# Kernel tuning notes

Hardware: AMD Instinct MI355X
Metric: run time of the kernel (lower is better)

## Reference

```python
import jax, jax.numpy as jnp
import numpy as np
import math

D_DIM = 512
N_HEAD = 8
HIDDEN = 2048
N_LAYERS = 4
CONTEXT = 64
MAX_LEN = 5000


def make_pe(d_model, max_len=MAX_LEN):
    position = np.arange(max_len)[:, None].astype(np.float32)
    div_term = np.exp(np.arange(0, d_model, 2).astype(np.float32) * (-math.log(10000.0) / d_model))
    pe = np.zeros((max_len, d_model), dtype=np.float32)
    pe[:, 0::2] = np.sin(position * div_term)
    pe[:, 1::2] = np.cos(position * div_term)
    return jnp.asarray(pe)


def setup_inputs() -> dict:
    key = jax.random.key(0)
    ks = jax.random.split(key, 64)
    B, T, IN = 16, 2048, 512
    inp = {}
    inp["trajectory"] = jax.random.normal(ks[0], (B, T, IN), dtype=jnp.float32)
    inp["obs_length"] = jax.random.randint(ks[1], (B,), 0, T)
    s = 0.02
    inp["w_in"] = jax.random.normal(ks[2], (IN, D_DIM), dtype=jnp.float32) * s
    inp["b_in"] = jnp.zeros((D_DIM,), dtype=jnp.float32)
    # per-layer params
    params = []
    ki = 3
    for l in range(N_LAYERS):
        p = {}
        p["w_qkv"] = jax.random.normal(ks[ki], (D_DIM, 3 * D_DIM), dtype=jnp.float32) * s; ki += 1
        p["b_qkv"] = jnp.zeros((3 * D_DIM,), dtype=jnp.float32)
        p["w_o"] = jax.random.normal(ks[ki], (D_DIM, D_DIM), dtype=jnp.float32) * s; ki += 1
        p["b_o"] = jnp.zeros((D_DIM,), dtype=jnp.float32)
        p["w_ff1"] = jax.random.normal(ks[ki], (D_DIM, HIDDEN), dtype=jnp.float32) * s; ki += 1
        p["b_ff1"] = jnp.zeros((HIDDEN,), dtype=jnp.float32)
        p["w_ff2"] = jax.random.normal(ks[ki], (HIDDEN, D_DIM), dtype=jnp.float32) * s; ki += 1
        p["b_ff2"] = jnp.zeros((D_DIM,), dtype=jnp.float32)
        p["ln1_g"] = jnp.ones((D_DIM,), dtype=jnp.float32)
        p["ln1_b"] = jnp.zeros((D_DIM,), dtype=jnp.float32)
        p["ln2_g"] = jnp.ones((D_DIM,), dtype=jnp.float32)
        p["ln2_b"] = jnp.zeros((D_DIM,), dtype=jnp.float32)
        for name, v in p.items():
            inp[f"L{l}_{name}"] = v
    return inp


def layer_norm(x, g, b, eps=1e-5):
    mu = jnp.mean(x, axis=-1, keepdims=True)
    var = jnp.mean((x - mu) ** 2, axis=-1, keepdims=True)
    return (x - mu) * jax.lax.rsqrt(var + eps) * g + b


def build_attn_mask(T, obs_length, context_length):
    # boolean mask, True = masked out. Causal + per-sample context window.
    i = jnp.arange(T)[:, None]
    j = jnp.arange(T)[None, :]
    causal = j > i  # (T, T)
    # window restriction applies for rows i with context_length < i < obs_length:
    # mask positions j <= i - context_length - 1, i.e. j < i - context_length
    window = j < (i - context_length)  # (T,T)
    row_active = (i[None, :, :] > context_length) & (i[None, :, :] < obs_length[:, None, None])  # (B,T,1)
    mask = causal[None] | (window[None] & row_active)  # (B,T,T)
    return mask


def encoder_layer(x, mask_add, pad_bool, p):
    B, T, D = x.shape
    H = N_HEAD
    Dh = D // H
    qkv = x @ p["w_qkv"] + p["b_qkv"]  # (B,T,3D)
    q, k, v = jnp.split(qkv, 3, axis=-1)
    q = q.reshape(B, T, H, Dh).transpose(0, 2, 1, 3)
    k = k.reshape(B, T, H, Dh).transpose(0, 2, 1, 3)
    v = v.reshape(B, T, H, Dh).transpose(0, 2, 1, 3)
    scores = jnp.einsum("bhqd,bhkd->bhqk", q, k) / jnp.sqrt(jnp.float32(Dh))
    scores = scores + mask_add[:, None] + pad_bool[:, None, None, :] * jnp.float32(-1e9)
    attn = jax.nn.softmax(scores, axis=-1)
    ctx = jnp.einsum("bhqk,bhkd->bhqd", attn, v)
    ctx = ctx.transpose(0, 2, 1, 3).reshape(B, T, D)
    attn_out = ctx @ p["w_o"] + p["b_o"]
    x = layer_norm(x + attn_out, p["ln1_g"], p["ln1_b"])
    ff = jax.nn.relu(x @ p["w_ff1"] + p["b_ff1"]) @ p["w_ff2"] + p["b_ff2"]
    x = layer_norm(x + ff, p["ln2_g"], p["ln2_b"])
    return x


def reference(trajectory, obs_length, w_in, b_in,
              L0_w_qkv, L0_b_qkv, L0_w_o, L0_b_o, L0_w_ff1, L0_b_ff1, L0_w_ff2, L0_b_ff2, L0_ln1_g, L0_ln1_b, L0_ln2_g, L0_ln2_b,
              L1_w_qkv, L1_b_qkv, L1_w_o, L1_b_o, L1_w_ff1, L1_b_ff1, L1_w_ff2, L1_b_ff2, L1_ln1_g, L1_ln1_b, L1_ln2_g, L1_ln2_b,
              L2_w_qkv, L2_b_qkv, L2_w_o, L2_b_o, L2_w_ff1, L2_b_ff1, L2_w_ff2, L2_b_ff2, L2_ln1_g, L2_ln1_b, L2_ln2_g, L2_ln2_b,
              L3_w_qkv, L3_b_qkv, L3_w_o, L3_b_o, L3_w_ff1, L3_b_ff1, L3_w_ff2, L3_b_ff2, L3_ln1_g, L3_ln1_b, L3_ln2_g, L3_ln2_b):
    B, T, _ = trajectory.shape
    pad = jnp.arange(T)[None, :] > obs_length[:, None]  # (B,T) True = pad
    x = trajectory @ w_in + b_in
    x = x + make_pe(D_DIM)[None, :T]
    mask_bool = build_attn_mask(T, obs_length, CONTEXT)  # (B,T,T)
    mask_add = jnp.where(mask_bool, jnp.float32(-1e9), jnp.float32(0.0))
    layers = [
        dict(w_qkv=L0_w_qkv, b_qkv=L0_b_qkv, w_o=L0_w_o, b_o=L0_b_o, w_ff1=L0_w_ff1, b_ff1=L0_b_ff1, w_ff2=L0_w_ff2, b_ff2=L0_b_ff2, ln1_g=L0_ln1_g, ln1_b=L0_ln1_b, ln2_g=L0_ln2_g, ln2_b=L0_ln2_b),
        dict(w_qkv=L1_w_qkv, b_qkv=L1_b_qkv, w_o=L1_w_o, b_o=L1_b_o, w_ff1=L1_w_ff1, b_ff1=L1_b_ff1, w_ff2=L1_w_ff2, b_ff2=L1_b_ff2, ln1_g=L1_ln1_g, ln1_b=L1_ln1_b, ln2_g=L1_ln2_g, ln2_b=L1_ln2_b),
        dict(w_qkv=L2_w_qkv, b_qkv=L2_b_qkv, w_o=L2_w_o, b_o=L2_b_o, w_ff1=L2_w_ff1, b_ff1=L2_b_ff1, w_ff2=L2_w_ff2, b_ff2=L2_b_ff2, ln1_g=L2_ln1_g, ln1_b=L2_ln1_b, ln2_g=L2_ln2_g, ln2_b=L2_ln2_b),
        dict(w_qkv=L3_w_qkv, b_qkv=L3_b_qkv, w_o=L3_w_o, b_o=L3_b_o, w_ff1=L3_w_ff1, b_ff1=L3_b_ff1, w_ff2=L3_w_ff2, b_ff2=L3_b_ff2, ln1_g=L3_ln1_g, ln1_b=L3_ln1_b, ln2_g=L3_ln2_g, ln2_b=L3_ln2_b),
    ]
    for p in layers:
        x = encoder_layer(x, mask_add, pad, p)
    # aggregate
    keep = ~pad
    x = x * keep[:, :, None]
    denom = jnp.sum(keep, axis=1).astype(x.dtype)[:, None]
    return jnp.sum(x, axis=1) / denom
```

## Files before the change

kernel.cpp:

```cpp
#include <hip/hip_runtime.h>

typedef unsigned short u16;
typedef unsigned int u32;
typedef __bf16 bf16x8 __attribute__((ext_vector_type(8)));
typedef float f32x4 __attribute__((ext_vector_type(4)));

#define MFMA16(a, b, c) __builtin_amdgcn_mfma_f32_16x16x32_bf16((a), (b), (c), 0, 0, 0)

__device__ __forceinline__ u16 f2bf(float x) {
    union { float f; u32 u; } v; v.f = x;
    u32 r = v.u + 0x7fffu + ((v.u >> 16) & 1u);
    return (u16)(r >> 16);
}
__device__ __forceinline__ float bf2f(u16 x) {
    union { u32 u; float f; } v; v.u = ((u32)x) << 16; return v.f;
}

typedef const __attribute__((address_space(1))) u32* gas1_t;
typedef __attribute__((address_space(3))) u32* las3_t;
__device__ __forceinline__ void g2lds16(const void* g, void* l) {
    __builtin_amdgcn_global_load_lds((gas1_t)g, (las3_t)l, 16, 0, 0);
}

template <int MODE>
__global__ __launch_bounds__(256) void gemm_bf16(
    const u16* __restrict__ A, const u16* __restrict__ BT,
    const float* __restrict__ bias, float* __restrict__ outF,
    u16* __restrict__ outB, const float* __restrict__ aux,
    const int* __restrict__ obs,
    int M, int N, int K)
{
    __shared__ u16 As[3][128 * 32];
    __shared__ u16 Bs[3][128 * 32];
    const int tid = threadIdx.x;
    const int w = tid >> 6, l = tid & 63;
    const int gx = gridDim.x, gy = gridDim.y;
    const int orig = blockIdx.y * gx + blockIdx.x;
    int tm, tn;
    if ((gy & 15) == 0) {
        const int xcd = orig & 7;
        const int loc = orig >> 3;
        tn = loc % gx;
        const int j = loc / gx;
        const int bb = j >> 1;
        tm = bb * 16 + ((xcd - bb) & 7) + ((j & 1) << 3);
    } else {
        tm = blockIdx.y; tn = blockIdx.x;
    }
    const int bm = tm * 128, bn = tn * 128;
    if ((bm & 2047) > obs[bm >> 11]) return;
    const int wr = (w >> 1) * 64, wc = (w & 1) * 64;
    f32x4 acc[4][4] = {};
    const int lane15 = l & 15, lhi = l >> 4;

    const int larow = l >> 2;
    const int lacol = (((l & 3) ^ ((l >> 3) & 3)) << 3);
    const int r0a = 16 * w, r0b = 16 * (w + 4);
    const u16* Ap = &A[(size_t)(bm + larow) * K + lacol];
    const u16* Bp = &BT[(size_t)(bn + larow) * K + lacol];

    auto STAGE = [&](int buf, int kt) {
        g2lds16(Ap + (size_t)r0a * K + kt, &As[buf][r0a * 32]);
        g2lds16(Bp + (size_t)r0a * K + kt, &Bs[buf][r0a * 32]);
        g2lds16(Ap + (size_t)r0b * K + kt, &As[buf][r0b * 32]);
        g2lds16(Bp + (size_t)r0b * K + kt, &Bs[buf][r0b * 32]);
    };

    const int nk = K >> 5;
    STAGE(0, 0);
    STAGE(1, 32);
    const int gsw = ((lhi ^ ((lane15 >> 1) & 3)) << 3);
    int cur = 0;
    for (int ki = 0; ki < nk; ++ki) {
        if (ki + 1 < nk) {
            asm volatile("s_waitcnt vmcnt(4)\n\ts_barrier" ::: "memory");
        } else {
            asm volatile("s_waitcnt vmcnt(0)\n\ts_barrier" ::: "memory");
        }
        if (ki + 2 < nk) {
            int tgt = cur + 2; if (tgt >= 3) tgt -= 3;
            STAGE(tgt, (ki + 2) << 5);
        }
        bf16x8 af[4], bfr[4];
        #pragma unroll
        for (int i = 0; i < 4; ++i)
            af[i] = *(const bf16x8*)&As[cur][(wr + i * 16 + lane15) * 32 + gsw];
        #pragma unroll
        for (int j = 0; j < 4; ++j)
            bfr[j] = *(const bf16x8*)&Bs[cur][(wc + j * 16 + lane15) * 32 + gsw];
        #pragma unroll
        for (int i = 0; i < 4; ++i)
            #pragma unroll
            for (int j = 0; j < 4; ++j)
                acc[i][j] = MFMA16(af[i], bfr[j], acc[i][j]);
        cur = (cur == 2) ? 0 : cur + 1;
    }

    const int r0 = bm + wr + lhi * 4;
    const int c0 = bn + wc + lane15;
    #pragma unroll
    for (int i = 0; i < 4; ++i) {
        #pragma unroll
        for (int j = 0; j < 4; ++j) {
            const int col = c0 + j * 16;
            const float bc = bias[col];
            #pragma unroll
            for (int r = 0; r < 4; ++r) {
                const int row = r0 + i * 16 + r;
                const size_t idx = (size_t)row * N + col;
                float val = acc[i][j][r] + bc;
                if constexpr (MODE == 0) {
                    val += aux[(size_t)(row & 2047) * 512 + col];
                    outF[idx] = val;
                    outB[idx] = f2bf(val);
                } else if constexpr (MODE == 1) {
                    outB[idx] = f2bf(val);
                } else if constexpr (MODE == 2) {
                    outF[idx] = val + aux[idx];
                } else {
                    outB[idx] = f2bf(fmaxf(val, 0.f));
                }
            }
        }
    }
}

__global__ void pe_kernel(float* __restrict__ PE) {
    const int idx = blockIdx.x * 256 + threadIdx.x;
    const int t = idx >> 8, p = idx & 255;
    const float fr = expf((float)(2 * p) * -0.017988946039015984f);
    const float arg = (float)t * fr;
    float s, c;
    sincosf(arg, &s, &c);
    float2 v = {s, c};
    *(float2*)&PE[(size_t)t * 512 + 2 * p] = v;
}

__global__ __launch_bounds__(256) void attn_kernel(
    const u16* __restrict__ QKV, u16* __restrict__ CTX, const int* __restrict__ obs,
    float* __restrict__ PBm, float* __restrict__ PBl, float* __restrict__ PBo)
{
    __shared__ u16 Ks[64 * 64];
    __shared__ u16 Vt[64 * 64];
    __shared__ u16 Ps[4][16 * 64];
    const int b = blockIdx.z, h = blockIdx.y;
    const int L = obs[b];
    const int tid = threadIdx.x, w = tid >> 6, l = tid & 63;
    const size_t tb = (size_t)b * 2048;

    if (blockIdx.x >= 32) {
        const int cbase = (blockIdx.x - 32) * 4;
        if (cbase * 64 > L) return;
        const int cc = cbase + w;
        float* pP = (float*)Ks;
        u16 q16[64];
        #pragma unroll
        for (int dd = 0; dd < 8; ++dd)
            *(uint4*)&q16[dd * 8] = *(const uint4*)&QKV[(tb + L) * 1536 + h * 64 + dd * 8];
        const int j = cc * 64 + l;
        const bool val = (j <= L);
        float s = -3.0e38f;
        if (val) {
            s = 0.f;
            const u16* kp = &QKV[(tb + j) * 1536 + 512 + h * 64];
            #pragma unroll
            for (int dd = 0; dd < 8; ++dd) {
                uint4 kk = *(const uint4*)&kp[dd * 8];
                const u16* ke = (const u16*)&kk;
                #pragma unroll
                for (int e = 0; e < 8; ++e)
                    s += bf2f(q16[dd * 8 + e]) * bf2f(ke[e]);
            }
            s *= 0.125f;
        }
        float mx = s;
        #pragma unroll
        for (int d = 1; d < 64; d <<= 1) mx = fmaxf(mx, __shfl_xor(mx, d, 64));
        const float p = val ? __expf(s - mx) : 0.f;
        float ps = p;
        #pragma unroll
        for (int d = 1; d < 64; d <<= 1) ps += __shfl_xor(ps, d, 64);
        pP[w * 64 + l] = p;
        __builtin_amdgcn_wave_barrier();
        if (cc * 64 <= L) {
            float oacc = 0.f;
            #pragma unroll 4
            for (int jj = 0; jj < 64; ++jj) {
                const int key = cc * 64 + jj;
                const int rr = (key <= L) ? key : L;
                oacc += pP[w * 64 + jj] * bf2f(QKV[(tb + rr) * 1536 + 1024 + h * 64 + l]);
            }
            const int pidx = (b * 8 + h) * 32 + cc;
            PBo[(size_t)pidx * 64 + l] = oacc;
            if (l == 0) { PBm[pidx] = mx; PBl[pidx] = ps; }
        }
        return;
    }

    const int i0 = blockIdx.x * 64;
    if (i0 > L) return;

    bf16x8 qa0, qa1;
    {
        const int qrow = i0 + 16 * w + (l & 15);
        const u16* qp = &QKV[(tb + qrow) * 1536 + h * 64];
        qa0 = *(const bf16x8*)(qp + 8 * (l >> 4));
        qa1 = *(const bf16x8*)(qp + 32 + 8 * (l >> 4));
    }
    const int g0 = (l >> 4) ^ (l & 7);
    const int g1 = ((l >> 4) + 4) ^ (l & 7);

    float m_r[4] = {-1e30f, -1e30f, -1e30f, -1e30f};
    float l_r[4] = {0.f, 0.f, 0.f, 0.f};
    f32x4 acc_o[4] = {};
    const int klo = (i0 >= 128) ? (i0 - 64) : 0;
    int khi = (L < klo) ? klo : min(i0 + 63, L);

    for (int j0 = klo; j0 <= khi; j0 += 64) {
        __syncthreads();
        {
            const int krow0 = 8 * w + (l >> 3);
            const int kswz = ((l & 7) ^ (l >> 3)) << 3;
            #pragma unroll
            for (int q = 0; q < 2; ++q) {
                const int row = krow0 + 32 * q;
                g2lds16(&QKV[(tb + j0 + row) * 1536 + 512 + h * 64 + kswz],
                        &Ks[(8 * w + 32 * q) * 64]);
            }
            const int vr = tid >> 3, c8 = (tid & 7) * 8;
            #pragma unroll
            for (int q = 0; q < 2; ++q) {
                const int row = vr + 32 * q;
                uint4 vv = *(const uint4*)&QKV[(tb + j0 + row) * 1536 + 1024 + h * 64 + c8];
                const u16* vs = (const u16*)&vv;
                #pragma unroll
                for (int e = 0; e < 8; ++e) {
                    const int d = c8 + e;
                    Vt[d * 64 + (((row >> 3) ^ e) << 3) + (row & 7)] = vs[e];
                }
            }
        }
        __syncthreads();
        f32x4 s[4];
        #pragma unroll
        for (int f = 0; f < 4; ++f) {
            f32x4 z = {0.f, 0.f, 0.f, 0.f};
            const int rowk = (f * 16 + (l & 15)) * 64;
            bf16x8 kb0 = *(const bf16x8*)&Ks[rowk + g0 * 8];
            bf16x8 kb1 = *(const bf16x8*)&Ks[rowk + g1 * 8];
            z = MFMA16(qa0, kb0, z);
            z = MFMA16(qa1, kb1, z);
            s[f] = z;
        }
        float pm[4];
        #pragma unroll
        for (int r = 0; r < 4; ++r) {
            const int i_r = i0 + 16 * w + (l >> 4) * 4 + r;
            float mx = -__builtin_inff();
            #pragma unroll
            for (int f = 0; f < 4; ++f) {
                const int j = j0 + f * 16 + (l & 15);
                float sv = s[f][r] * 0.125f;
                const bool ok = (i_r >= L) ? (j == klo)
                              : (j <= i_r && (i_r <= 64 || j >= i_r - 64));
                sv = ok ? sv : -__builtin_inff();
                s[f][r] = sv;
                mx = fmaxf(mx, sv);
            }
            pm[r] = mx;
        }
        #pragma unroll
        for (int d = 1; d < 16; d <<= 1)
            #pragma unroll
            for (int r = 0; r < 4; ++r) pm[r] = fmaxf(pm[r], __shfl_xor(pm[r], d, 64));
        float sc[4];
        #pragma unroll
        for (int r = 0; r < 4; ++r) {
            const float mn = fmaxf(m_r[r], fmaxf(pm[r], -1e30f));
            sc[r] = __expf(m_r[r] - mn);
            m_r[r] = mn;
            l_r[r] *= sc[r];
        }
        #pragma unroll
        for (int f = 0; f < 4; ++f)
            #pragma unroll
            for (int r = 0; r < 4; ++r) acc_o[f][r] *= sc[r];
        float ps[4] = {0.f, 0.f, 0.f, 0.f};
        #pragma unroll
        for (int f = 0; f < 4; ++f)
            #pragma unroll
            for (int r = 0; r < 4; ++r) {
                const float p = __expf(s[f][r] - m_r[r]);
                s[f][r] = p;
                ps[r] += p;
            }
        #pragma unroll
        for (int d = 1; d < 16; d <<= 1)
            #pragma unroll
            for (int r = 0; r < 4; ++r) ps[r] += __shfl_xor(ps[r], d, 64);
        #pragma unroll
        for (int r = 0; r < 4; ++r) l_r[r] += ps[r];
        {
            const int cg = ((l >> 3) & 1);
            #pragma unroll
            for (int f = 0; f < 4; ++f)
                #pragma unroll
                for (int r = 0; r < 4; ++r) {
                    const int prow = (l >> 4) * 4 + r;
                    Ps[w][prow * 64 + (((f * 2 + cg) ^ (prow & 7)) << 3) + (l & 7)] =
                        f2bf(s[f][r]);
                }
        }
        bf16x8 pa0 = *(const bf16x8*)&Ps[w][(l & 15) * 64 + g0 * 8];
        bf16x8 pa1 = *(const bf16x8*)&Ps[w][(l & 15) * 64 + g1 * 8];
        #pragma unroll
        for (int f = 0; f < 4; ++f) {
            const int dv = (f * 16 + (l & 15)) * 64;
            bf16x8 vb0 = *(const bf16x8*)&Vt[dv + g0 * 8];
            bf16x8 vb1 = *(const bf16x8*)&Vt[dv + g1 * 8];
            acc_o[f] = MFMA16(pa0, vb0, acc_o[f]);
            acc_o[f] = MFMA16(pa1, vb1, acc_o[f]);
        }
    }
    #pragma unroll
    for (int r = 0; r < 4; ++r) {
        const float inv = 1.f / l_r[r];
        const int row = i0 + 16 * w + (l >> 4) * 4 + r;
        if (row != L) {
            #pragma unroll
            for (int f = 0; f < 4; ++f)
                CTX[(tb + row) * 512 + h * 64 + f * 16 + (l & 15)] = f2bf(acc_o[f][r] * inv);
        }
    }
}

__global__ void attn_merge(const float* __restrict__ PBm, const float* __restrict__ PBl,
                           const float* __restrict__ PBo, u16* __restrict__ CTX,
                           const int* __restrict__ obs)
{
    const int h = blockIdx.x, b = blockIdx.y, l = threadIdx.x;
    const int L = obs[b];
    const int nc = (L >> 6) + 1;
    const int base = (b * 8 + h) * 32;
    float m = -3.0e38f;
    for (int c = 0; c < nc; ++c) m = fmaxf(m, PBm[base + c]);
    float lt = 0.f, ot = 0.f;
    for (int c = 0; c < nc; ++c) {
        const float sc = __expf(PBm[base + c] - m);
        lt += sc * PBl[base + c];
        ot += sc * PBo[(size_t)(base + c) * 64 + l];
    }
    CTX[((size_t)b * 2048 + L) * 512 + h * 64 + l] = f2bf(ot / lt);
}

__global__ __launch_bounds__(256) void ln_kernel(
    const float* __restrict__ Y, const float* __restrict__ gw,
    const float* __restrict__ bw, float* __restrict__ X, u16* __restrict__ Xb,
    const int* __restrict__ obs)
{
    const int tok0 = blockIdx.x * 4;
    if ((tok0 & 2047) > obs[tok0 >> 11]) return;
    const int tok = tok0 + (threadIdx.x >> 6);
    const int l = threadIdx.x & 63;
    const float* y = &Y[(size_t)tok * 512 + l * 8];
    f32x4 v0 = *(const f32x4*)y;
    f32x4 v1 = *(const f32x4*)(y + 4);
    float s = 0.f, sq = 0.f;
    #pragma unroll
    for (int e = 0; e < 4; ++e) {
        s += v0[e] + v1[e];
        sq += v0[e] * v0[e] + v1[e] * v1[e];
    }
    #pragma unroll
    for (int d = 1; d < 64; d <<= 1) {
        s += __shfl_xor(s, d, 64);
        sq += __shfl_xor(sq, d, 64);
    }
    const float mean = s * (1.f / 512.f);
    const float var = sq * (1.f / 512.f) - mean * mean;
    const float rstd = rsqrtf(var + 1e-5f);
    f32x4 o0, o1;
    union { u16 us[8]; uint4 u4; } pk;
    #pragma unroll
    for (int e = 0; e < 8; ++e) {
        const int d = l * 8 + e;
        const float xv = (e < 4) ? v0[e] : v1[e - 4];
        const float ov = (xv - mean) * rstd * gw[d] + bw[d];
        if (e < 4) o0[e] = ov; else o1[e - 4] = ov;
        pk.us[e] = f2bf(ov);
    }
    float* xo = &X[(size_t)tok * 512 + l * 8];
    *(f32x4*)xo = o0;
    *(f32x4*)(xo + 4) = o1;
    *(uint4*)&Xb[(size_t)tok * 512 + l * 8] = pk.u4;
}

__global__ void cast_bf16_kernel(const float* __restrict__ in, u16* __restrict__ out, int n) {
    const int i = (blockIdx.x * 256 + threadIdx.x) * 4;
    if (i + 3 < n) {
        f32x4 v = *(const f32x4*)&in[i];
        union { u16 us[4]; uint2 u2; } pk;
        #pragma unroll
        for (int e = 0; e < 4; ++e) pk.us[e] = f2bf(v[e]);
        *(uint2*)&out[i] = pk.u2;
    }
}

__global__ void transpose_cast(const float* __restrict__ W, u16* __restrict__ WT, int K, int N) {
    __shared__ float t[32][33];
    const int n0 = blockIdx.x * 32, k0 = blockIdx.y * 32;
    const int tx = threadIdx.x, ty = threadIdx.y;
    #pragma unroll
    for (int r = 0; r < 32; r += 8)
        t[ty + r][tx] = W[(size_t)(k0 + ty + r) * N + n0 + tx];
    __syncthreads();
    #pragma unroll
    for (int r = 0; r < 32; r += 8)
        WT[(size_t)(n0 + ty + r) * K + k0 + tx] = f2bf(t[tx][ty + r]);
}

struct WPack { const float* src[16]; u16* dst[16]; };
__global__ void transpose_all(WPack p) {
    __shared__ float t[32][33];
    int id = blockIdx.x;
    const int lyr = id / 3072;
    id -= lyr * 3072;
    int wi, K, N;
    if (id < 768)       { wi = 0; K = 512;  N = 1536; }
    else if (id < 1024) { wi = 1; K = 512;  N = 512;  id -= 768; }
    else if (id < 2048) { wi = 2; K = 512;  N = 2048; id -= 1024; }
    else                { wi = 3; K = 2048; N = 512;  id -= 2048; }
    const float* W = p.src[lyr * 4 + wi];
    u16* D = p.dst[lyr * 4 + wi];
    const int nx = N >> 5;
    const int n0 = (id % nx) * 32, k0 = (id / nx) * 32;
    const int tx = threadIdx.x, ty = threadIdx.y;
    #pragma unroll
    for (int r = 0; r < 32; r += 8)
        t[ty + r][tx] = W[(size_t)(k0 + ty + r) * N + n0 + tx];
    __syncthreads();
    #pragma unroll
    for (int r = 0; r < 32; r += 8)
        D[(size_t)(n0 + ty + r) * K + k0 + tx] = f2bf(t[tx][ty + r]);
}

__global__ void agg_partial(const float* __restrict__ X, float* __restrict__ part,
                            const int* __restrict__ obs) {
    const int b = blockIdx.y, c = blockIdx.x, d = threadIdx.x;
    const int L = obs[b];
    float s = 0.f;
    const int t0 = c * 128;
    int tend = t0 + 128;
    if (tend > L + 1) tend = L + 1;
    for (int t = t0; t < tend; ++t) s += X[((size_t)b * 2048 + t) * 512 + d];
    part[((size_t)b * 16 + c) * 512 + d] = s;
}

__global__ void agg_final(const float* __restrict__ part, float* __restrict__ out,
                          const int* __restrict__ obs) {
    const int b = blockIdx.x, d = threadIdx.x;
    float s = 0.f;
    #pragma unroll
    for (int c = 0; c < 16; ++c) s += part[((size_t)b * 16 + c) * 512 + d];
    out[b * 512 + d] = s / (float)(obs[b] + 1);
}

extern "C" void kernel_launch(void* const* d_in, const int* in_sizes, int n_in,
                              void* d_out, int out_size, void* d_ws, size_t ws_size,
                              hipStream_t stream)
{
    const int M = 32768;
    const int FCH = 16384;
    const bool bigws = ws_size >= (size_t)270 * 1024 * 1024;
    const float* traj = (const float*)d_in[0];
    const int* obs = (const int*)d_in[1];
    const float* w_in = (const float*)d_in[2];
    const float* b_in = (const float*)d_in[3];

    char* base = (char*)d_ws;
    size_t off = 0;
    auto carve = [&](size_t bytes) -> void* {
        void* p = base + off;
        off += (bytes + 255) & ~(size_t)255;
        return p;
    };
    u16* U     = (u16*)carve((size_t)M * (bigws ? 2048 : 1536) * 2);
    u16* Xb    = (u16*)carve((size_t)M * 512 * 2);
    float* X   = (float*)carve((size_t)M * 512 * 4);
    float* PE  = (float*)carve((size_t)2048 * 512 * 4);
    float* PBm = (float*)carve((size_t)16 * 8 * 32 * 4);
    float* PBl = (float*)carve((size_t)16 * 8 * 32 * 4);
    float* PBo = (float*)carve((size_t)16 * 8 * 32 * 64 * 4);
    float* part = (float*)carve((size_t)16 * 16 * 512 * 4);
    u16* wTin  = (u16*)carve((size_t)512 * 512 * 2);
    u16 *wqkv[4], *wo[4], *wff1[4], *wff2[4];
    for (int l = 0; l < 4; ++l) {
        wqkv[l] = (u16*)carve((size_t)1536 * 512 * 2);
        wo[l]   = (u16*)carve((size_t)512 * 512 * 2);
        wff1[l] = (u16*)carve((size_t)2048 * 512 * 2);
        wff2[l] = (u16*)carve((size_t)512 * 2048 * 2);
    }

    dim3 tb32(32, 8);
    pe_kernel<<<2048, 256, 0, stream>>>(PE);
    transpose_cast<<<dim3(16, 16), tb32, 0, stream>>>(w_in, wTin, 512, 512);
    {
        WPack p;
        for (int l = 0; l < 4; ++l) {
            const int bi = 4 + 12 * l;
            p.src[l * 4 + 0] = (const float*)d_in[bi + 0];
            p.src[l * 4 + 1] = (const float*)d_in[bi + 2];
            p.src[l * 4 + 2] = (const float*)d_in[bi + 4];
            p.src[l * 4 + 3] = (const float*)d_in[bi + 6];
            p.dst[l * 4 + 0] = wqkv[l];
            p.dst[l * 4 + 1] = wo[l];
            p.dst[l * 4 + 2] = wff1[l];
            p.dst[l * 4 + 3] = wff2[l];
        }
        transpose_all<<<12288, tb32, 0, stream>>>(p);
    }

    cast_bf16_kernel<<<(M * 512) / 1024, 256, 0, stream>>>(traj, U, M * 512);
    gemm_bf16<0><<<dim3(4, M / 128), 256, 0, stream>>>(
        U, wTin, b_in, X, Xb, PE, obs, M, 512, 512);

    for (int lyr = 0; lyr < 4; ++lyr) {
        const int bi = 4 + 12 * lyr;
        const float* b_qkv = (const float*)d_in[bi + 1];
        const float* b_o   = (const float*)d_in[bi + 3];
        const float* b_ff1 = (const float*)d_in[bi + 5];
        const float* b_ff2 = (const float*)d_in[bi + 7];
        const float* ln1g  = (const float*)d_in[bi + 8];
        const float* ln1b  = (const float*)d_in[bi + 9];
        const float* ln2g  = (const float*)d_in[bi + 10];
        const float* ln2b  = (const float*)d_in[bi + 11];

        gemm_bf16<1><<<dim3(12, M / 128), 256, 0, stream>>>(
            Xb, wqkv[lyr], b_qkv, nullptr, U, nullptr, obs, M, 1536, 512);
        attn_kernel<<<dim3(40, 8, 16), 256, 0, stream>>>(U, Xb, obs, PBm, PBl, PBo);
        attn_merge<<<dim3(8, 16), 64, 0, stream>>>(PBm, PBl, PBo, Xb, obs);
        gemm_bf16<2><<<dim3(4, M / 128), 256, 0, stream>>>(
            Xb, wo[lyr], b_o, X, nullptr, X, obs, M, 512, 512);
        ln_kernel<<<M / 4, 256, 0, stream>>>(X, ln1g, ln1b, X, Xb, obs);
        if (bigws) {
            gemm_bf16<3><<<dim3(16, M / 128), 256, 0, stream>>>(
                Xb, wff1[lyr], b_ff1, nullptr, U, nullptr, obs, M, 2048, 512);
            gemm_bf16<2><<<dim3(4, M / 128), 256, 0, stream>>>(
                U, wff2[lyr], b_ff2, X, nullptr, X, obs, M, 512, 2048);
        } else {
            for (int c = 0; c < 2; ++c) {
                gemm_bf16<3><<<dim3(16, FCH / 128), 256, 0, stream>>>(
                    Xb + (size_t)c * FCH * 512, wff1[lyr], b_ff1, nullptr, U, nullptr,
                    obs + c * 8, FCH, 2048, 512);
                gemm_bf16<2><<<dim3(4, FCH / 128), 256, 0, stream>>>(
                    U, wff2[lyr], b_ff2, X + (size_t)c * FCH * 512, nullptr,
                    X + (size_t)c * FCH * 512, obs + c * 8, FCH, 512, 2048);
            }
        }
        ln_kernel<<<M / 4, 256, 0, stream>>>(X, ln2g, ln2b, X, Xb, obs);
    }

    agg_partial<<<dim3(16, 16), 512, 0, stream>>>(X, part, obs);
    agg_final<<<16, 512, 0, stream>>>(part, (float*)d_out, obs);
}
```

Measured before the change: 1.345 ms.

## Specialize GEMM pipeline depth per shape and skip padded-row casts

Adds a DEEP template parameter to the bf16 GEMM. Narrow-N GEMMs (N=512: input projection, output projection, FF2) get a 5-buffer LDS pipeline with 4 stages in flight. Wide-N GEMMs (QKV, FF1) get a simple double-buffered loop with an unswizzled LDS layout. The deeper pipeline is meant to hide load latency where few blocks are launched, and the smaller buffer is meant to raise occupancy on the wide launches, at the risk of LDS bank conflicts on the unswizzled path. The input cast kernel also skips tokens beyond each sample's observed length, which the GEMM already ignores.

Result: no change. 1.329 ms, median of 3 (-1.2%).

```diff
diff --git a/kernel.cpp b/kernel.cpp
--- a/kernel.cpp
+++ b/kernel.cpp
@@ -22,7 +22,7 @@
     __builtin_amdgcn_global_load_lds((gas1_t)g, (las3_t)l, 16, 0, 0);
 }
 
-template <int MODE>
+template <int MODE, int DEEP>
 __global__ __launch_bounds__(256) void gemm_bf16(
     const u16* __restrict__ A, const u16* __restrict__ BT,
     const float* __restrict__ bias, float* __restrict__ outF,
@@ -30,8 +30,9 @@
     const int* __restrict__ obs,
     int M, int N, int K)
 {
-    __shared__ u16 As[3][128 * 32];
-    __shared__ u16 Bs[3][128 * 32];
+    constexpr int NBUF = DEEP ? 5 : 2;
+    __shared__ u16 As[NBUF][128 * 32];
+    __shared__ u16 Bs[NBUF][128 * 32];
     const int tid = threadIdx.x;
     const int w = tid >> 6, l = tid & 63;
     const int gx = gridDim.x, gy = gridDim.y;
@@ -54,7 +55,8 @@
     const int lane15 = l & 15, lhi = l >> 4;
 
     const int larow = l >> 2;
-    const int lacol = (((l & 3) ^ ((l >> 3) & 3)) << 3);
+    const int lacol = DEEP ? (((l & 3) ^ ((l >> 3) & 3)) << 3) : ((l & 3) << 3);
+    const int gsw   = DEEP ? ((lhi ^ ((lane15 >> 1) & 3)) << 3) : (lhi << 3);
     const int r0a = 16 * w, r0b = 16 * (w + 4);
     const u16* Ap = &A[(size_t)(bm + larow) * K + lacol];
     const u16* Bp = &BT[(size_t)(bn + larow) * K + lacol];
@@ -65,35 +67,49 @@
         g2lds16(Ap + (size_t)r0b * K + kt, &As[buf][r0b * 32]);
         g2lds16(Bp + (size_t)r0b * K + kt, &Bs[buf][r0b * 32]);
     };
-
-    const int nk = K >> 5;
-    STAGE(0, 0);
-    STAGE(1, 32);
-    const int gsw = ((lhi ^ ((lane15 >> 1) & 3)) << 3);
-    int cur = 0;
-    for (int ki = 0; ki < nk; ++ki) {
-        if (ki + 1 < nk) {
-            asm volatile("s_waitcnt vmcnt(4)\n\ts_barrier" ::: "memory");
-        } else {
-            asm volatile("s_waitcnt vmcnt(0)\n\ts_barrier" ::: "memory");
-        }
-        if (ki + 2 < nk) {
-            int tgt = cur + 2; if (tgt >= 3) tgt -= 3;
-            STAGE(tgt, (ki + 2) << 5);
-        }
+    auto COMPUTE = [&](int buf) {
         bf16x8 af[4], bfr[4];
         #pragma unroll
         for (int i = 0; i < 4; ++i)
-            af[i] = *(const bf16x8*)&As[cur][(wr + i * 16 + lane15) * 32 + gsw];
+            af[i] = *(const bf16x8*)&As[buf][(wr + i * 16 + lane15) * 32 + gsw];
         #pragma unroll
         for (int j = 0; j < 4; ++j)
-            bfr[j] = *(const bf16x8*)&Bs[cur][(wc + j * 16 + lane15) * 32 + gsw];
+            bfr[j] = *(const bf16x8*)&Bs[buf][(wc + j * 16 + lane15) * 32 + gsw];
         #pragma unroll
         for (int i = 0; i < 4; ++i)
             #pragma unroll
             for (int j = 0; j < 4; ++j)
                 acc[i][j] = MFMA16(af[i], bfr[j], acc[i][j]);
-        cur = (cur == 2) ? 0 : cur + 1;
+    };
+
+    const int nk = K >> 5;
+    if constexpr (!DEEP) {
+        STAGE(0, 0);
+        __syncthreads();
+        int cur = 0;
+        for (int ki = 0; ki < nk; ++ki) {
+            if (ki + 1 < nk) STAGE(cur ^ 1, (ki + 1) << 5);
+            COMPUTE(cur);
+            __syncthreads();
+            cur ^= 1;
+        }
+    } else {
+        #pragma unroll
+        for (int b = 0; b < 4; ++b) STAGE(b, b << 5);
+        int cur = 0;
+        for (int ki = 0; ki < nk; ++ki) {
+            const int rem = nk - 1 - ki;
+            if (rem >= 3)      asm volatile("s_waitcnt vmcnt(12)\n\ts_barrier" ::: "memory");
+            else if (rem == 2) asm volatile("s_waitcnt vmcnt(8)\n\ts_barrier" ::: "memory");
+            else if (rem == 1) asm volatile("s_waitcnt vmcnt(4)\n\ts_barrier" ::: "memory");
+            else               asm volatile("s_waitcnt vmcnt(0)\n\ts_barrier" ::: "memory");
+            if (ki + 4 < nk) {
+                int tgt = cur + 4; if (tgt >= 5) tgt -= 5;
+                STAGE(tgt, (ki + 4) << 5);
+            }
+            COMPUTE(cur);
+            cur = (cur == 4) ? 0 : cur + 1;
+        }
     }
 
     const int r0 = bm + wr + lhi * 4;
@@ -395,8 +411,11 @@
     *(uint4*)&Xb[(size_t)tok * 512 + l * 8] = pk.u4;
 }
 
-__global__ void cast_bf16_kernel(const float* __restrict__ in, u16* __restrict__ out, int n) {
+__global__ void cast_bf16_kernel(const float* __restrict__ in, u16* __restrict__ out,
+                                 const int* __restrict__ obs, int n) {
     const int i = (blockIdx.x * 256 + threadIdx.x) * 4;
+    const int tok0 = (blockIdx.x * 1024) >> 9;
+    if ((tok0 & 2047) > obs[tok0 >> 11]) return;
     if (i + 3 < n) {
         f32x4 v = *(const f32x4*)&in[i];
         union { u16 us[4]; uint2 u2; } pk;
@@ -520,8 +539,8 @@
         transpose_all<<<12288, tb32, 0, stream>>>(p);
     }
 
-    cast_bf16_kernel<<<(M * 512) / 1024, 256, 0, stream>>>(traj, U, M * 512);
-    gemm_bf16<0><<<dim3(4, M / 128), 256, 0, stream>>>(
+    cast_bf16_kernel<<<(M * 512) / 1024, 256, 0, stream>>>(traj, U, obs, M * 512);
+    gemm_bf16<0, 1><<<dim3(4, M / 128), 256, 0, stream>>>(
         U, wTin, b_in, X, Xb, PE, obs, M, 512, 512);
 
     for (int lyr = 0; lyr < 4; ++lyr) {
@@ -535,24 +554,24 @@
         const float* ln2g  = (const float*)d_in[bi + 10];
         const float* ln2b  = (const float*)d_in[bi + 11];
 
-        gemm_bf16<1><<<dim3(12, M / 128), 256, 0, stream>>>(
+        gemm_bf16<1, 0><<<dim3(12, M / 128), 256, 0, stream>>>(
             Xb, wqkv[lyr], b_qkv, nullptr, U, nullptr, obs, M, 1536, 512);
         attn_kernel<<<dim3(40, 8, 16), 256, 0, stream>>>(U, Xb, obs, PBm, PBl, PBo);
         attn_merge<<<dim3(8, 16), 64, 0, stream>>>(PBm, PBl, PBo, Xb, obs);
-        gemm_bf16<2><<<dim3(4, M / 128), 256, 0, stream>>>(
+        gemm_bf16<2, 1><<<dim3(4, M / 128), 256, 0, stream>>>(
             Xb, wo[lyr], b_o, X, nullptr, X, obs, M, 512, 512);
         ln_kernel<<<M / 4, 256, 0, stream>>>(X, ln1g, ln1b, X, Xb, obs);
         if (bigws) {
-            gemm_bf16<3><<<dim3(16, M / 128), 256, 0, stream>>>(
+            gemm_bf16<3, 0><<<dim3(16, M / 128), 256, 0, stream>>>(
                 Xb, wff1[lyr], b_ff1, nullptr, U, nullptr, obs, M, 2048, 512);
-            gemm_bf16<2><<<dim3(4, M / 128), 256, 0, stream>>>(
+            gemm_bf16<2, 1><<<dim3(4, M / 128), 256, 0, stream>>>(
                 U, wff2[lyr], b_ff2, X, nullptr, X, obs, M, 512, 2048);
         } else {
             for (int c = 0; c < 2; ++c) {
-                gemm_bf16<3><<<dim3(16, FCH / 128), 256, 0, stream>>>(
+                gemm_bf16<3, 0><<<dim3(16, FCH / 128), 256, 0, stream>>>(
                     Xb + (size_t)c * FCH * 512, wff1[lyr], b_ff1, nullptr, U, nullptr,
                     obs + c * 8, FCH, 2048, 512);
-                gemm_bf16<2><<<dim3(4, FCH / 128), 256, 0, stream>>>(
+                gemm_bf16<2, 1><<<dim3(4, FCH / 128), 256, 0, stream>>>(
                     U, wff2[lyr], b_ff2, X + (size_t)c * FCH * 512, nullptr,
                     X + (size_t)c * FCH * 512, obs + c * 8, FCH, 512, 2048);
             }
```
